# Optimization experiments

Measured on AMD Instinct MI355X. Metric: run time of the kernel, lower is better.

## Reference

```python
import jax, jax.numpy as jnp
import numpy as np

V_NODES = 50000


def _spmm(vals, rows, cols, m):
    # sparse (V,V) @ dense (V, F): gather source rows, scale, scatter-add to dest rows
    return jax.ops.segment_sum(vals[:, None] * m[cols], rows, num_segments=V_NODES)


def setup_inputs() -> dict:
    key = jax.random.key(0)
    ks = jax.random.split(key, 6)
    B, Cin, Cout, K, V, E = 4, 128, 128, 5, V_NODES, 800000
    x = jax.random.normal(ks[0], (B, Cin, V), dtype=jnp.float32)
    # random symmetric-normalized-laplacian-like values (scaled so recurrence stays bounded)
    lap_vals = jax.random.normal(ks[1], (E,), dtype=jnp.float32) * 0.05
    fan_in = Cin  # kaiming_normal_ mode='fan_in' on (K, Cin, Cout): fan_in = Cin
    weight = jax.random.normal(ks[2], (K, Cin, Cout), dtype=jnp.float32) * np.sqrt(2.0 / fan_in)
    bias = jnp.full((Cout,), 0.01, dtype=jnp.float32)
    lap_rows = jax.random.randint(ks[3], (E,), 0, V, dtype=jnp.int32)
    lap_cols = jax.random.randint(ks[4], (E,), 0, V, dtype=jnp.int32)
    return {"x": x, "lap_vals": lap_vals, "weight": weight, "bias": bias,
            "lap_rows": lap_rows, "lap_cols": lap_cols}


def reference(x, lap_vals, weight, bias, lap_rows, lap_cols):
    B, Cin, V = x.shape
    K, _, Cout = weight.shape
    # (B, Cin, V) -> (V, B*Cin)
    x0 = jnp.transpose(x, (2, 0, 1)).reshape(V, B * Cin)

    def contract(xk, k):
        # accumulate order-k contribution: (V, B, Cin) x (Cin, Cout) -> (V, B, Cout)
        return jnp.einsum('vbi,io->vbo', xk.reshape(V, B, Cin), weight[k])

    out = contract(x0, 0)
    if K > 1:
        x1 = _spmm(lap_vals, lap_rows, lap_cols, x0)
        out = out + contract(x1, 1)
        for k in range(2, K):
            x2 = 2.0 * _spmm(lap_vals, lap_rows, lap_cols, x1) - x0
            out = out + contract(x2, k)
            x0, x1 = x1, x2
    out = out + bias  # broadcast over (V, B, Cout)
    # (V, B, Cout) -> (B, Cout, V)
    return jnp.transpose(out, (1, 2, 0))
```

## Files before the change

### kernel.cpp

```cpp
#include <hip/hip_runtime.h>

#define V_NODES 50000
#define FDIM    512
#define CIN     128
#define COUT    128
#define BATCH   4
#define KORD    5
#define KTOT    (KORD * CIN)
#define SCAN_NBLK ((V_NODES + 255) / 256)
#define VBLKS   ((V_NODES + 255) / 256)
#define TQ_BLOCKS (VBLKS * (FDIM / 64))
#define CONVW_BLOCKS ((KORD * COUT + 3) / 4)

typedef float f32x4 __attribute__((ext_vector_type(4)));
typedef int   i32x4 __attribute__((ext_vector_type(4)));

struct EPair { float w; int c; };

__global__ __launch_bounds__(256) void prep1_kernel(const float* __restrict__ x,
                                                    float* __restrict__ sc0,
                                                    float* __restrict__ invsc,
                                                    const int* __restrict__ rows,
                                                    int* __restrict__ cnt,
                                                    int E, int histBlocks,
                                                    const float* __restrict__ W,
                                                    signed char* __restrict__ Wq8,
                                                    float* __restrict__ Wsc) {
    const int bid = blockIdx.x;
    if (bid < VBLKS) {
        const int v = bid * 256 + threadIdx.x;
        if (v >= V_NODES) return;
        const float* xp = x + v;
        float m0 = 0.f, m1 = 0.f, m2 = 0.f, m3 = 0.f;
        #pragma unroll 4
        for (int r = 0; r < FDIM; r += 4) {
            m0 = fmaxf(m0, fabsf(xp[(size_t)(r + 0) * V_NODES]));
            m1 = fmaxf(m1, fabsf(xp[(size_t)(r + 1) * V_NODES]));
            m2 = fmaxf(m2, fabsf(xp[(size_t)(r + 2) * V_NODES]));
            m3 = fmaxf(m3, fabsf(xp[(size_t)(r + 3) * V_NODES]));
        }
        float m = fmaxf(fmaxf(m0, m1), fmaxf(m2, m3));
        sc0[v] = m / 127.f;
        invsc[v] = (m > 0.f) ? 127.f / m : 0.f;
    } else if (bid < VBLKS + histBlocks) {
        int e = (bid - VBLKS) * 256 + threadIdx.x;
        if (e < E) atomicAdd(&cnt[rows[e]], 1);
    } else {
        const int g = (bid - VBLKS - histBlocks) * 4 + (threadIdx.x >> 6);
        if (g >= KORD * COUT) return;
        const int co = g & 127;
        const int ord = g >> 7;
        const int lane = threadIdx.x & 63;
        float w0 = W[(size_t)(ord * 128 + lane * 2 + 0) * COUT + co];
        float w1 = W[(size_t)(ord * 128 + lane * 2 + 1) * COUT + co];
        float m = fmaxf(fabsf(w0), fabsf(w1));
        #pragma unroll
        for (int off = 1; off < 64; off <<= 1) m = fmaxf(m, __shfl_xor(m, off, 64));
        float inv = (m > 0.f) ? 127.f / m : 0.f;
        int q0 = max(-127, min(127, (int)rintf(w0 * inv)));
        int q1 = max(-127, min(127, (int)rintf(w1 * inv)));
        unsigned short pk = (unsigned short)((q0 & 0xff) | ((q1 & 0xff) << 8));
        *(unsigned short*)(Wq8 + (size_t)co * KTOT + ord * 128 + lane * 2) = pk;
        if (lane == 0) Wsc[ord * 128 + co] = m / 127.f;
    }
}

__global__ __launch_bounds__(256) void scan1_kernel(const int* __restrict__ cnt,
                                                    int* __restrict__ rowPtr,
                                                    int* __restrict__ blkSum) {
    __shared__ int sh[256];
    const int t = threadIdx.x;
    const int i = blockIdx.x * 256 + t;
    int v = (i < V_NODES) ? cnt[i] : 0;
    sh[t] = v;
    __syncthreads();
    #pragma unroll
    for (int off = 1; off < 256; off <<= 1) {
        int u = (t >= off) ? sh[t - off] : 0;
        __syncthreads();
        sh[t] += u;
        __syncthreads();
    }
    if (i < V_NODES) rowPtr[i] = sh[t] - v;
    if (t == 255) blkSum[blockIdx.x] = sh[255];
}

__global__ __launch_bounds__(256) void scan23_kernel(const int* __restrict__ blkSum,
                                                     int* __restrict__ rowPtr,
                                                     int* __restrict__ cursor) {
    __shared__ int sh[256];
    const int t = threadIdx.x;
    int v = (t < SCAN_NBLK) ? blkSum[t] : 0;
    sh[t] = v;
    __syncthreads();
    #pragma unroll
    for (int off = 1; off < 256; off <<= 1) {
        int u = (t >= off) ? sh[t - off] : 0;
        __syncthreads();
        sh[t] += u;
        __syncthreads();
    }
    const int boff = sh[blockIdx.x] - blkSum[blockIdx.x];
    const int i = blockIdx.x * 256 + t;
    if (i < V_NODES) {
        int r = rowPtr[i] + boff;
        rowPtr[i] = r;
        cursor[i] = r;
    }
    if (blockIdx.x == 0 && t == 255) rowPtr[V_NODES] = sh[255];
}

__global__ __launch_bounds__(256) void prep2_kernel(const float* __restrict__ x,
                                                    const float* __restrict__ invsc,
                                                    signed char* __restrict__ xi,
                                                    const float* __restrict__ vals,
                                                    const int* __restrict__ rows,
                                                    const int* __restrict__ cols,
                                                    int* __restrict__ cursor,
                                                    EPair* __restrict__ ep, int E) {
    __shared__ signed char lds[256 * 80];
    const int bid = blockIdx.x;
    if (bid < TQ_BLOCKS) {
        const int vb = bid % VBLKS;
        const int rb = bid / VBLKS;
        const int v0 = vb * 256, r0 = rb * 64;
        const int t = threadIdx.x;
        const int lane = t & 63, w = t >> 6;
        int vbase = v0 + lane * 4;
        if (vbase > V_NODES - 4) vbase = V_NODES - 4;
        const f32x4 inv = *(const f32x4*)(invsc + vbase);
        const int vv = lane * 4;
        #pragma unroll
        for (int i = 0; i < 16; ++i) {
            const int r = r0 + w * 16 + i;
            f32x4 xv = *(const f32x4*)(x + (size_t)r * V_NODES + vbase);
            #pragma unroll
            for (int j = 0; j < 4; ++j) {
                int q = (int)rintf(xv[j] * inv[j]);
                q = max(-127, min(127, q));
                lds[(vv + j) * 80 + w * 16 + i] = (signed char)q;
            }
        }
        __syncthreads();
        #pragma unroll
        for (int it = 0; it < 4; ++it) {
            int flat = it * 256 + t;
            int vl = flat >> 2, c = flat & 3;
            int v = v0 + vl;
            if (v < V_NODES) {
                uint4 val = *(const uint4*)(lds + vl * 80 + c * 16);
                *(uint4*)(xi + (size_t)v * FDIM + r0 + c * 16) = val;
            }
        }
    } else {
        int e = (bid - TQ_BLOCKS) * 256 + threadIdx.x;
        if (e >= E) return;
        int r = rows[e];
        int pos = atomicAdd(&cursor[r], 1);
        EPair p; p.w = vals[e]; p.c = cols[e];
        ep[pos] = p;
    }
}

__global__ __launch_bounds__(256) void spmm_i8_kernel(const EPair* __restrict__ ep,
                                                      const int* __restrict__ rowPtr,
                                                      const signed char* __restrict__ xi,
                                                      const float* __restrict__ xsc,
                                                      const signed char* __restrict__ oldi,
                                                      const float* __restrict__ oldsc,
                                                      signed char* __restrict__ yi,
                                                      float* __restrict__ ysc,
                                                      float alpha, int beta) {
    const int wid = threadIdx.x >> 6;
    const int lane = threadIdx.x & 63;
    const int row = blockIdx.x * 4 + wid;
    if (row >= V_NODES) return;
    const int s = rowPtr[row], e_end = rowPtr[row + 1];
    const uint2* __restrict__ xq = (const uint2*)xi;

    float acc[8];
    #pragma unroll
    for (int j = 0; j < 8; ++j) acc[j] = 0.f;

    int e = s;
    for (; e + 3 < e_end; e += 4) {
        EPair p[4];
        #pragma unroll
        for (int i = 0; i < 4; ++i) p[i] = ep[e + i];
        float w[4];
        #pragma unroll
        for (int i = 0; i < 4; ++i) w[i] = p[i].w * xsc[p[i].c];
        uint2 q[4];
        #pragma unroll
        for (int i = 0; i < 4; ++i) q[i] = xq[(size_t)p[i].c * 64 + lane];
        #pragma unroll
        for (int i = 0; i < 4; ++i) {
            #pragma unroll
            for (int wd = 0; wd < 2; ++wd) {
                unsigned int uu = wd ? q[i].y : q[i].x;
                #pragma unroll
                for (int b = 0; b < 4; ++b) {
                    float xv = (float)((signed char)(uu >> (8 * b)));
                    acc[wd * 4 + b] += w[i] * xv;
                }
            }
        }
    }
    for (; e < e_end; ++e) {
        EPair p0 = ep[e];
        float w0 = p0.w * xsc[p0.c];
        uint2 q0 = xq[(size_t)p0.c * 64 + lane];
        #pragma unroll
        for (int wd = 0; wd < 2; ++wd) {
            unsigned int uu = wd ? q0.y : q0.x;
            #pragma unroll
            for (int b = 0; b < 4; ++b) {
                float xv = (float)((signed char)(uu >> (8 * b)));
                acc[wd * 4 + b] += w0 * xv;
            }
        }
    }

    float r[8];
    #pragma unroll
    for (int j = 0; j < 8; ++j) r[j] = alpha * acc[j];
    if (beta) {
        uint2 q = ((const uint2*)oldi)[(size_t)row * 64 + lane];
        const float os = oldsc[row];
        #pragma unroll
        for (int wd = 0; wd < 2; ++wd) {
            unsigned int uu = wd ? q.y : q.x;
            #pragma unroll
            for (int b = 0; b < 4; ++b)
                r[wd * 4 + b] -= os * (float)((signed char)(uu >> (8 * b)));
        }
    }

    float m = 0.f;
    #pragma unroll
    for (int j = 0; j < 8; ++j) m = fmaxf(m, fabsf(r[j]));
    #pragma unroll
    for (int off = 1; off < 64; off <<= 1) m = fmaxf(m, __shfl_xor(m, off, 64));
    float inv = (m > 0.f) ? 127.f / m : 0.f;
    unsigned int ow[2] = {0u, 0u};
    #pragma unroll
    for (int j = 0; j < 8; ++j) {
        int si = (int)rintf(r[j] * inv);
        si = max(-127, min(127, si));
        ow[j >> 2] |= ((unsigned int)(si & 0xff)) << (8 * (j & 3));
    }
    uint2 oi; oi.x = ow[0]; oi.y = ow[1];
    ((uint2*)yi)[(size_t)row * 64 + lane] = oi;
    if (lane == 0) ysc[row] = m / 127.f;
}

__global__ __launch_bounds__(512) void gemm_mfma_kernel(const signed char* __restrict__ Ti8,
                                                        const float* __restrict__ Tsc,
                                                        const signed char* __restrict__ Wq8,
                                                        const float* __restrict__ Wsc,
                                                        const float* __restrict__ bias,
                                                        float* __restrict__ out) {
    __shared__ signed char Abuf[3][128 * 64];
    const int tid = threadIdx.x;
    const int lane = tid & 63;
    const int wid = tid >> 6;
    const int wr = wid >> 2;
    const int wc = wid & 3;
    const int v0 = blockIdx.x * 128;
    const int b = blockIdx.y;
    const int lr = lane & 15;
    const int lk = lane >> 4;

    size_t gof;
    {
        int rl = tid >> 2;
        int ch = tid & 3;
        int rowg = v0 + rl;
        if (rowg >= V_NODES) rowg = V_NODES - 1;
        int srcch = (ch - ((rl >> 1) & 3)) & 3;
        gof = (size_t)rowg * FDIM + b * CIN + (size_t)(srcch << 4);
    }

    f32x4 accF[4][2];
    i32x4 accI[4][2];
    #pragma unroll
    for (int mf = 0; mf < 4; ++mf)
        #pragma unroll
        for (int nf = 0; nf < 2; ++nf) {
            accF[mf][nf] = (f32x4){0.f, 0.f, 0.f, 0.f};
            accI[mf][nf] = (i32x4){0, 0, 0, 0};
        }

    const signed char* Bb = Wq8 + (size_t)(wc * 32 + lr) * KTOT + lk * 16;

    #pragma unroll
    for (int st = 0; st < 2; ++st) {
        const size_t soff = (size_t)(st & 1) * 64;
        __builtin_amdgcn_global_load_lds(
            (const __attribute__((address_space(1))) void*)(Ti8 + gof + soff),
            (__attribute__((address_space(3))) void*)(&Abuf[st][tid * 16]),
            16, 0, 0);
    }
    i32x4 bcur[2];
    #pragma unroll
    for (int nf = 0; nf < 2; ++nf)
        bcur[nf] = *(const i32x4*)(Bb + (size_t)nf * 16 * KTOT);
    f32x4 sv[4];
    float swv0 = 0.f, swv1 = 0.f;
    asm volatile("s_waitcnt vmcnt(0)" ::: "memory");
    asm volatile("s_barrier" ::: "memory");

    int curm = 0, stm = 2;
    #pragma unroll 1
    for (int s = 0; s < 10; ++s) {
        i32x4 bnxt[2];
        if (s < 9) {
            #pragma unroll
            for (int nf = 0; nf < 2; ++nf)
                bnxt[nf] = *(const i32x4*)(Bb + (size_t)nf * 16 * KTOT + (s + 1) * 64);
        }
        if (!(s & 1)) {
            const int ord = s >> 1;
            #pragma unroll
            for (int mf = 0; mf < 4; ++mf) {
                int base = v0 + wr * 64 + mf * 16 + lk * 4;
                if (base > V_NODES - 4) base = V_NODES - 4;
                sv[mf] = *(const f32x4*)(Tsc + (size_t)ord * V_NODES + base);
            }
            swv0 = Wsc[ord * 128 + wc * 32 + lr];
            swv1 = Wsc[ord * 128 + wc * 32 + 16 + lr];
        }
        __builtin_amdgcn_sched_barrier(0);
        if (s < 8) {
            const int sn = s + 2;
            const size_t soff = (size_t)(sn >> 1) * ((size_t)V_NODES * FDIM) + (size_t)((sn & 1) * 64);
            __builtin_amdgcn_global_load_lds(
                (const __attribute__((address_space(1))) void*)(Ti8 + gof + soff),
                (__attribute__((address_space(3))) void*)(&Abuf[stm][tid * 16]),
                16, 0, 0);
        }
        const signed char* Ab = &Abuf[curm][0];
        i32x4 a[4];
        #pragma unroll
        for (int mf = 0; mf < 4; ++mf) {
            int rl = wr * 64 + mf * 16 + lr;
            int phys = rl * 64 + (((lk + (rl >> 1)) & 3) << 4);
            a[mf] = *(const i32x4*)(Ab + phys);
        }
        #pragma unroll
        for (int mf = 0; mf < 4; ++mf)
            #pragma unroll
            for (int nf = 0; nf < 2; ++nf)
                accI[mf][nf] = __builtin_amdgcn_mfma_i32_16x16x64_i8(a[mf], bcur[nf], accI[mf][nf], 0, 0, 0);
        if (s & 1) {
            #pragma unroll
            for (int mf = 0; mf < 4; ++mf)
                #pragma unroll
                for (int nf = 0; nf < 2; ++nf) {
                    float sw = nf ? swv1 : swv0;
                    #pragma unroll
                    for (int e = 0; e < 4; ++e)
                        accF[mf][nf][e] += (float)accI[mf][nf][e] * (sv[mf][e] * sw);
                    accI[mf][nf] = (i32x4){0, 0, 0, 0};
                }
        }
        if (s < 9) {
            bcur[0] = bnxt[0];
            bcur[1] = bnxt[1];
        }
        asm volatile("s_barrier" ::: "memory");
        curm = (curm == 2) ? 0 : curm + 1;
        stm  = (stm == 2) ? 0 : stm + 1;
    }

    float* lds_f = (float*)&Abuf[0][0];
    const float bs0 = bias[wc * 32 + lr];
    const float bs1 = bias[wc * 32 + 16 + lr];
    #pragma unroll
    for (int p = 0; p < 4; ++p) {
        if (wc == p) {
            #pragma unroll
            for (int mf = 0; mf < 4; ++mf)
                #pragma unroll
                for (int nf = 0; nf < 2; ++nf) {
                    int co_l = nf * 16 + lr;
                    int vbase = wr * 64 + mf * 16 + lk * 4;
                    f32x4 val = accF[mf][nf];
                    float bs = nf ? bs1 : bs0;
                    val[0] += bs; val[1] += bs; val[2] += bs; val[3] += bs;
                    *(f32x4*)(lds_f + co_l * 132 + vbase) = val;
                }
        }
        __syncthreads();
        #pragma unroll
        for (int i = 0; i < 2; ++i) {
            int flat = i * 512 + tid;
            int co_l = flat >> 5;
            int v4 = flat & 31;
            int v = v0 + v4 * 4;
            if (v < V_NODES) {
                f32x4 val = *(const f32x4*)(lds_f + co_l * 132 + v4 * 4);
                *(f32x4*)(out + (size_t)(b * COUT + p * 32 + co_l) * V_NODES + v) = val;
            }
        }
        __syncthreads();
    }
}

extern "C" void kernel_launch(void* const* d_in, const int* in_sizes, int n_in,
                              void* d_out, int out_size, void* d_ws, size_t ws_size,
                              hipStream_t stream) {
    const float* x    = (const float*)d_in[0];
    const float* vals = (const float*)d_in[1];
    const float* W    = (const float*)d_in[2];
    const float* bias = (const float*)d_in[3];
    const int* rows   = (const int*)d_in[4];
    const int* cols   = (const int*)d_in[5];
    const int E = in_sizes[1];
    float* out = (float*)d_out;

    signed char* i8T = (signed char*)d_ws;
    float* sc  = (float*)(i8T + (size_t)KORD * V_NODES * FDIM);
    float* invsc = sc + (size_t)KORD * V_NODES + 64;
    signed char* Wq8 = (signed char*)(invsc + V_NODES + 64);
    float* Wsc = (float*)(Wq8 + (size_t)COUT * KTOT);
    EPair* ep     = (EPair*)(Wsc + KORD * COUT);
    int*   rowPtr = (int*)(ep + E);
    int*   cursor = rowPtr + V_NODES + 1;
    int*   cnt    = cursor + V_NODES;
    int*   blkSum = cnt + V_NODES;

    signed char* i8T0 = i8T;
    signed char* i8T1 = i8T + 1 * (size_t)V_NODES * FDIM;
    signed char* i8T2 = i8T + 2 * (size_t)V_NODES * FDIM;
    signed char* i8T3 = i8T + 3 * (size_t)V_NODES * FDIM;
    signed char* i8T4 = i8T + 4 * (size_t)V_NODES * FDIM;
    float* sc0 = sc + 0 * (size_t)V_NODES;
    float* sc1 = sc + 1 * (size_t)V_NODES;
    float* sc2 = sc + 2 * (size_t)V_NODES;
    float* sc3 = sc + 3 * (size_t)V_NODES;
    float* sc4 = sc + 4 * (size_t)V_NODES;

    const int histBlocks = (E + 255) / 256;
    const int spB4 = (V_NODES + 3) / 4;

    hipMemsetAsync(cnt, 0, V_NODES * sizeof(int), stream);
    prep1_kernel<<<VBLKS + histBlocks + CONVW_BLOCKS, 256, 0, stream>>>(
        x, sc0, invsc, rows, cnt, E, histBlocks, W, Wq8, Wsc);
    scan1_kernel<<<SCAN_NBLK, 256, 0, stream>>>(cnt, rowPtr, blkSum);
    scan23_kernel<<<SCAN_NBLK, 256, 0, stream>>>(blkSum, rowPtr, cursor);
    prep2_kernel<<<TQ_BLOCKS + histBlocks, 256, 0, stream>>>(
        x, invsc, i8T0, vals, rows, cols, cursor, ep, E);

    spmm_i8_kernel<<<spB4, 256, 0, stream>>>(ep, rowPtr, i8T0, sc0, i8T0, sc0, i8T1, sc1, 1.f, 0);
    spmm_i8_kernel<<<spB4, 256, 0, stream>>>(ep, rowPtr, i8T1, sc1, i8T0, sc0, i8T2, sc2, 2.f, 1);
    spmm_i8_kernel<<<spB4, 256, 0, stream>>>(ep, rowPtr, i8T2, sc2, i8T1, sc1, i8T3, sc3, 2.f, 1);
    spmm_i8_kernel<<<spB4, 256, 0, stream>>>(ep, rowPtr, i8T3, sc3, i8T2, sc2, i8T4, sc4, 2.f, 1);

    dim3 gg((V_NODES + 127) / 128, BATCH);
    gemm_mfma_kernel<<<gg, 512, 0, stream>>>(i8T, sc, Wq8, Wsc, bias, out);
}
```

Baseline: 492.2 us.

## Fuse x absmax into quantize pass with per-64-channel chunk scales

Removes the separate strided pass over x that computed a per-node absmax, and instead computes the max inside the transpose-quantize blocks, one scale per 64-channel chunk (8 scales per node for order 0). The SpMM and GEMM kernels are updated to read chunked scales for order 0, and the GEMM now applies scales after every 64-wide k-step rather than once per 128-channel order. The goal is to avoid reading the full fp32 x twice. The cost is more scale loads and float conversions in the GEMM inner loop, and a changed quantization granularity.

```diff
diff --git a/kernel.cpp b/kernel.cpp
--- a/kernel.cpp
+++ b/kernel.cpp
@@ -17,36 +17,18 @@
 
 struct EPair { float w; int c; };
 
-__global__ __launch_bounds__(256) void prep1_kernel(const float* __restrict__ x,
-                                                    float* __restrict__ sc0,
-                                                    float* __restrict__ invsc,
-                                                    const int* __restrict__ rows,
+__global__ __launch_bounds__(256) void prep1_kernel(const int* __restrict__ rows,
                                                     int* __restrict__ cnt,
                                                     int E, int histBlocks,
                                                     const float* __restrict__ W,
                                                     signed char* __restrict__ Wq8,
                                                     float* __restrict__ Wsc) {
     const int bid = blockIdx.x;
-    if (bid < VBLKS) {
-        const int v = bid * 256 + threadIdx.x;
-        if (v >= V_NODES) return;
-        const float* xp = x + v;
-        float m0 = 0.f, m1 = 0.f, m2 = 0.f, m3 = 0.f;
-        #pragma unroll 4
-        for (int r = 0; r < FDIM; r += 4) {
-            m0 = fmaxf(m0, fabsf(xp[(size_t)(r + 0) * V_NODES]));
-            m1 = fmaxf(m1, fabsf(xp[(size_t)(r + 1) * V_NODES]));
-            m2 = fmaxf(m2, fabsf(xp[(size_t)(r + 2) * V_NODES]));
-            m3 = fmaxf(m3, fabsf(xp[(size_t)(r + 3) * V_NODES]));
-        }
-        float m = fmaxf(fmaxf(m0, m1), fmaxf(m2, m3));
-        sc0[v] = m / 127.f;
-        invsc[v] = (m > 0.f) ? 127.f / m : 0.f;
-    } else if (bid < VBLKS + histBlocks) {
-        int e = (bid - VBLKS) * 256 + threadIdx.x;
+    if (bid < histBlocks) {
+        int e = bid * 256 + threadIdx.x;
         if (e < E) atomicAdd(&cnt[rows[e]], 1);
     } else {
-        const int g = (bid - VBLKS - histBlocks) * 4 + (threadIdx.x >> 6);
+        const int g = (bid - histBlocks) * 4 + (threadIdx.x >> 6);
         if (g >= KORD * COUT) return;
         const int co = g & 127;
         const int ord = g >> 7;
@@ -111,14 +93,15 @@
 }
 
 __global__ __launch_bounds__(256) void prep2_kernel(const float* __restrict__ x,
-                                                    const float* __restrict__ invsc,
                                                     signed char* __restrict__ xi,
+                                                    float* __restrict__ scChunk,
                                                     const float* __restrict__ vals,
                                                     const int* __restrict__ rows,
                                                     const int* __restrict__ cols,
                                                     int* __restrict__ cursor,
                                                     EPair* __restrict__ ep, int E) {
     __shared__ signed char lds[256 * 80];
+    __shared__ float red[4][256];
     const int bid = blockIdx.x;
     if (bid < TQ_BLOCKS) {
         const int vb = bid % VBLKS;
@@ -128,8 +111,26 @@
         const int lane = t & 63, w = t >> 6;
         int vbase = v0 + lane * 4;
         if (vbase > V_NODES - 4) vbase = V_NODES - 4;
-        const f32x4 inv = *(const f32x4*)(invsc + vbase);
         const int vv = lane * 4;
+        f32x4 m = (f32x4){0.f, 0.f, 0.f, 0.f};
+        #pragma unroll
+        for (int i = 0; i < 16; ++i) {
+            const int r = r0 + w * 16 + i;
+            f32x4 xv = *(const f32x4*)(x + (size_t)r * V_NODES + vbase);
+            #pragma unroll
+            for (int j = 0; j < 4; ++j) m[j] = fmaxf(m[j], fabsf(xv[j]));
+        }
+        #pragma unroll
+        for (int j = 0; j < 4; ++j) red[w][vv + j] = m[j];
+        __syncthreads();
+        f32x4 inv;
+        #pragma unroll
+        for (int j = 0; j < 4; ++j) {
+            float mm = fmaxf(fmaxf(red[0][vv + j], red[1][vv + j]),
+                             fmaxf(red[2][vv + j], red[3][vv + j]));
+            inv[j] = (mm > 0.f) ? 127.f / mm : 0.f;
+            if (w == 0) scChunk[(size_t)rb * V_NODES + vbase + j] = mm / 127.f;
+        }
         #pragma unroll
         for (int i = 0; i < 16; ++i) {
             const int r = r0 + w * 16 + i;
@@ -149,7 +150,7 @@
             int v = v0 + vl;
             if (v < V_NODES) {
                 uint4 val = *(const uint4*)(lds + vl * 80 + c * 16);
-                *(uint4*)(xi + (size_t)v * FDIM + r0 + c * 16) = val;
+                *(uint4*)(xi + (size_t)v * FDIM + r0 * 1 + c * 16 + 0) = val;
             }
         }
     } else {
@@ -161,6 +162,7 @@
         ep[pos] = p;
     }
 }
+
 
 __global__ __launch_bounds__(256) void spmm_i8_kernel(const EPair* __restrict__ ep,
                                                       const int* __restrict__ rowPtr,
@@ -170,13 +172,16 @@
                                                       const float* __restrict__ oldsc,
                                                       signed char* __restrict__ yi,
                                                       float* __restrict__ ysc,
-                                                      float alpha, int beta) {
+                                                      float alpha, int beta,
+                                                      int xChunked, int oldChunked) {
     const int wid = threadIdx.x >> 6;
     const int lane = threadIdx.x & 63;
     const int row = blockIdx.x * 4 + wid;
     if (row >= V_NODES) return;
     const int s = rowPtr[row], e_end = rowPtr[row + 1];
     const uint2* __restrict__ xq = (const uint2*)xi;
+    const float* __restrict__ xscl = xsc + (xChunked ? (size_t)(lane >> 3) * V_NODES : 0);
+    const float* __restrict__ oscl = oldsc + (oldChunked ? (size_t)(lane >> 3) * V_NODES : 0);
 
     float acc[8];
     #pragma unroll
@@ -189,7 +194,7 @@
         for (int i = 0; i < 4; ++i) p[i] = ep[e + i];
         float w[4];
         #pragma unroll
-        for (int i = 0; i < 4; ++i) w[i] = p[i].w * xsc[p[i].c];
+        for (int i = 0; i < 4; ++i) w[i] = p[i].w * xscl[p[i].c];
         uint2 q[4];
         #pragma unroll
         for (int i = 0; i < 4; ++i) q[i] = xq[(size_t)p[i].c * 64 + lane];
@@ -208,7 +213,7 @@
     }
     for (; e < e_end; ++e) {
         EPair p0 = ep[e];
-        float w0 = p0.w * xsc[p0.c];
+        float w0 = p0.w * xscl[p0.c];
         uint2 q0 = xq[(size_t)p0.c * 64 + lane];
         #pragma unroll
         for (int wd = 0; wd < 2; ++wd) {
@@ -226,7 +231,7 @@
     for (int j = 0; j < 8; ++j) r[j] = alpha * acc[j];
     if (beta) {
         uint2 q = ((const uint2*)oldi)[(size_t)row * 64 + lane];
-        const float os = oldsc[row];
+        const float os = oscl[row];
         #pragma unroll
         for (int wd = 0; wd < 2; ++wd) {
             unsigned int uu = wd ? q.y : q.x;
@@ -282,14 +287,11 @@
     }
 
     f32x4 accF[4][2];
-    i32x4 accI[4][2];
     #pragma unroll
     for (int mf = 0; mf < 4; ++mf)
         #pragma unroll
-        for (int nf = 0; nf < 2; ++nf) {
+        for (int nf = 0; nf < 2; ++nf)
             accF[mf][nf] = (f32x4){0.f, 0.f, 0.f, 0.f};
-            accI[mf][nf] = (i32x4){0, 0, 0, 0};
-        }
 
     const signed char* Bb = Wq8 + (size_t)(wc * 32 + lr) * KTOT + lk * 16;
 
@@ -305,30 +307,30 @@
     #pragma unroll
     for (int nf = 0; nf < 2; ++nf)
         bcur[nf] = *(const i32x4*)(Bb + (size_t)nf * 16 * KTOT);
-    f32x4 sv[4];
-    float swv0 = 0.f, swv1 = 0.f;
     asm volatile("s_waitcnt vmcnt(0)" ::: "memory");
     asm volatile("s_barrier" ::: "memory");
 
     int curm = 0, stm = 2;
     #pragma unroll 1
     for (int s = 0; s < 10; ++s) {
+        const int ord = s >> 1;
+        const float* svp = (ord == 0)
+            ? (Tsc + (size_t)(b * 2 + (s & 1)) * V_NODES)
+            : (Tsc + (size_t)(7 + ord) * V_NODES);
+        f32x4 sv[4];
+        #pragma unroll
+        for (int mf = 0; mf < 4; ++mf) {
+            int base = v0 + wr * 64 + mf * 16 + lk * 4;
+            if (base > V_NODES - 4) base = V_NODES - 4;
+            sv[mf] = *(const f32x4*)(svp + base);
+        }
+        float swv0 = Wsc[ord * 128 + wc * 32 + lr];
+        float swv1 = Wsc[ord * 128 + wc * 32 + 16 + lr];
         i32x4 bnxt[2];
         if (s < 9) {
             #pragma unroll
             for (int nf = 0; nf < 2; ++nf)
                 bnxt[nf] = *(const i32x4*)(Bb + (size_t)nf * 16 * KTOT + (s + 1) * 64);
-        }
-        if (!(s & 1)) {
-            const int ord = s >> 1;
-            #pragma unroll
-            for (int mf = 0; mf < 4; ++mf) {
-                int base = v0 + wr * 64 + mf * 16 + lk * 4;
-                if (base > V_NODES - 4) base = V_NODES - 4;
-                sv[mf] = *(const f32x4*)(Tsc + (size_t)ord * V_NODES + base);
-            }
-            swv0 = Wsc[ord * 128 + wc * 32 + lr];
-            swv1 = Wsc[ord * 128 + wc * 32 + 16 + lr];
         }
         __builtin_amdgcn_sched_barrier(0);
         if (s < 8) {
@@ -347,23 +349,17 @@
             int phys = rl * 64 + (((lk + (rl >> 1)) & 3) << 4);
             a[mf] = *(const i32x4*)(Ab + phys);
         }
+        const i32x4 zero = (i32x4){0, 0, 0, 0};
         #pragma unroll
         for (int mf = 0; mf < 4; ++mf)
             #pragma unroll
-            for (int nf = 0; nf < 2; ++nf)
-                accI[mf][nf] = __builtin_amdgcn_mfma_i32_16x16x64_i8(a[mf], bcur[nf], accI[mf][nf], 0, 0, 0);
-        if (s & 1) {
-            #pragma unroll
-            for (int mf = 0; mf < 4; ++mf)
+            for (int nf = 0; nf < 2; ++nf) {
+                i32x4 r = __builtin_amdgcn_mfma_i32_16x16x64_i8(a[mf], bcur[nf], zero, 0, 0, 0);
+                float sw = nf ? swv1 : swv0;
                 #pragma unroll
-                for (int nf = 0; nf < 2; ++nf) {
-                    float sw = nf ? swv1 : swv0;
-                    #pragma unroll
-                    for (int e = 0; e < 4; ++e)
-                        accF[mf][nf][e] += (float)accI[mf][nf][e] * (sv[mf][e] * sw);
-                    accI[mf][nf] = (i32x4){0, 0, 0, 0};
-                }
-        }
+                for (int e = 0; e < 4; ++e)
+                    accF[mf][nf][e] += (float)r[e] * (sv[mf][e] * sw);
+            }
         if (s < 9) {
             bcur[0] = bnxt[0];
             bcur[1] = bnxt[1];
@@ -420,9 +416,8 @@
     float* out = (float*)d_out;
 
     signed char* i8T = (signed char*)d_ws;
-    float* sc  = (float*)(i8T + (size_t)KORD * V_NODES * FDIM);
-    float* invsc = sc + (size_t)KORD * V_NODES + 64;
-    signed char* Wq8 = (signed char*)(invsc + V_NODES + 64);
+    float* Tsc = (float*)(i8T + (size_t)KORD * V_NODES * FDIM);
+    signed char* Wq8 = (signed char*)(Tsc + 12 * (size_t)V_NODES + 64);
     float* Wsc = (float*)(Wq8 + (size_t)COUT * KTOT);
     EPair* ep     = (EPair*)(Wsc + KORD * COUT);
     int*   rowPtr = (int*)(ep + E);
@@ -435,28 +430,28 @@
     signed char* i8T2 = i8T + 2 * (size_t)V_NODES * FDIM;
     signed char* i8T3 = i8T + 3 * (size_t)V_NODES * FDIM;
     signed char* i8T4 = i8T + 4 * (size_t)V_NODES * FDIM;
-    float* sc0 = sc + 0 * (size_t)V_NODES;
-    float* sc1 = sc + 1 * (size_t)V_NODES;
-    float* sc2 = sc + 2 * (size_t)V_NODES;
-    float* sc3 = sc + 3 * (size_t)V_NODES;
-    float* sc4 = sc + 4 * (size_t)V_NODES;
+    float* scC = Tsc;
+    float* sc1 = Tsc + 8 * (size_t)V_NODES;
+    float* sc2 = Tsc + 9 * (size_t)V_NODES;
+    float* sc3 = Tsc + 10 * (size_t)V_NODES;
+    float* sc4 = Tsc + 11 * (size_t)V_NODES;
 
     const int histBlocks = (E + 255) / 256;
     const int spB4 = (V_NODES + 3) / 4;
 
     hipMemsetAsync(cnt, 0, V_NODES * sizeof(int), stream);
-    prep1_kernel<<<VBLKS + histBlocks + CONVW_BLOCKS, 256, 0, stream>>>(
-        x, sc0, invsc, rows, cnt, E, histBlocks, W, Wq8, Wsc);
+    prep1_kernel<<<histBlocks + CONVW_BLOCKS, 256, 0, stream>>>(
+        rows, cnt, E, histBlocks, W, Wq8, Wsc);
     scan1_kernel<<<SCAN_NBLK, 256, 0, stream>>>(cnt, rowPtr, blkSum);
     scan23_kernel<<<SCAN_NBLK, 256, 0, stream>>>(blkSum, rowPtr, cursor);
     prep2_kernel<<<TQ_BLOCKS + histBlocks, 256, 0, stream>>>(
-        x, invsc, i8T0, vals, rows, cols, cursor, ep, E);
-
-    spmm_i8_kernel<<<spB4, 256, 0, stream>>>(ep, rowPtr, i8T0, sc0, i8T0, sc0, i8T1, sc1, 1.f, 0);
-    spmm_i8_kernel<<<spB4, 256, 0, stream>>>(ep, rowPtr, i8T1, sc1, i8T0, sc0, i8T2, sc2, 2.f, 1);
-    spmm_i8_kernel<<<spB4, 256, 0, stream>>>(ep, rowPtr, i8T2, sc2, i8T1, sc1, i8T3, sc3, 2.f, 1);
-    spmm_i8_kernel<<<spB4, 256, 0, stream>>>(ep, rowPtr, i8T3, sc3, i8T2, sc2, i8T4, sc4, 2.f, 1);
+        x, i8T0, scC, vals, rows, cols, cursor, ep, E);
+
+    spmm_i8_kernel<<<spB4, 256, 0, stream>>>(ep, rowPtr, i8T0, scC, i8T0, scC, i8T1, sc1, 1.f, 0, 1, 0);
+    spmm_i8_kernel<<<spB4, 256, 0, stream>>>(ep, rowPtr, i8T1, sc1, i8T0, scC, i8T2, sc2, 2.f, 1, 0, 1);
+    spmm_i8_kernel<<<spB4, 256, 0, stream>>>(ep, rowPtr, i8T2, sc2, i8T1, sc1, i8T3, sc3, 2.f, 1, 0, 0);
+    spmm_i8_kernel<<<spB4, 256, 0, stream>>>(ep, rowPtr, i8T3, sc3, i8T2, sc2, i8T4, sc4, 2.f, 1, 0, 0);
 
     dim3 gg((V_NODES + 127) / 128, BATCH);
-    gemm_mfma_kernel<<<gg, 512, 0, stream>>>(i8T, sc, Wq8, Wsc, bias, out);
-}
+    gemm_mfma_kernel<<<gg, 512, 0, stream>>>(i8T, Tsc, Wq8, Wsc, bias, out);
+}
```

Result: faster. 471.3 us (-4.3%).
